# Performance work log

Measured on AMD Instinct MI355X. Metric: run time of the kernel, lower is better.

The kernel has to match this reference:

```python
import jax, jax.numpy as jnp
import numpy as np

B, H, W, C = 64, 56, 56, 192
HEADS, WS, SS, MLP = 6, 7, 3, 768
N = WS * WS            # 49 tokens per window
NW = (H // WS) * (W // WS)  # 64 windows per image
HEAD_DIM = C // HEADS
SCALE = HEAD_DIM ** (-0.5)


def _rpi(ws):
    # relative position index, (N, N) int
    coords = np.stack(np.meshgrid(np.arange(ws), np.arange(ws), indexing='ij')).reshape(2, -1)
    rel = (coords[:, :, None] - coords[:, None, :]).transpose(1, 2, 0)
    rel[:, :, 0] += ws - 1
    rel[:, :, 1] += ws - 1
    rel[:, :, 0] *= 2 * ws - 1
    return rel.sum(-1)

RPI = _rpi(WS).reshape(-1)  # (N*N,)


def _attn_mask():
    # additive shift mask, (NW, N, N)
    label = np.zeros((H, W))
    cnt = 0
    slices = (slice(0, -WS), slice(-WS, -SS), slice(-SS, None))
    for hs in slices:
        for ws_ in slices:
            label[hs, ws_] = cnt
            cnt += 1
    lab = label.reshape(H // WS, WS, W // WS, WS).transpose(0, 2, 1, 3).reshape(NW, N)
    diff = lab[:, None, :] - lab[:, :, None]
    return np.where(diff != 0, -100.0, 0.0).astype(np.float32)

MASK = jnp.asarray(_attn_mask())  # (NW, N, N)


def _ln(t, g, b, eps=1e-5):
    m = jnp.mean(t, -1, keepdims=True)
    v = jnp.mean((t - m) ** 2, -1, keepdims=True)
    return (t - m) * jax.lax.rsqrt(v + eps) * g + b


def setup_inputs() -> dict:
    key = jax.random.key(0)
    ks = jax.random.split(key, 6)
    s = 0.02
    return {
        'x': jax.random.normal(ks[0], (B, H * W, C), jnp.float32),
        'ln1_g': jnp.ones((C,), jnp.float32),
        'ln1_b': jnp.zeros((C,), jnp.float32),
        'qkv_w': jax.random.normal(ks[1], (C, 3 * C), jnp.float32) * s,
        'qkv_b': jnp.zeros((3 * C,), jnp.float32),
        'proj_w': jax.random.normal(ks[2], (C, C), jnp.float32) * s,
        'proj_b': jnp.zeros((C,), jnp.float32),
        'rpb': jax.random.normal(ks[3], ((2 * WS - 1) ** 2, HEADS), jnp.float32) * s,
        'ln2_g': jnp.ones((C,), jnp.float32),
        'ln2_b': jnp.zeros((C,), jnp.float32),
        'mlp_w1': jax.random.normal(ks[4], (C, MLP), jnp.float32) * s,
        'mlp_b1': jnp.zeros((MLP,), jnp.float32),
        'mlp_w2': jax.random.normal(ks[5], (MLP, C), jnp.float32) * s,
        'mlp_b2': jnp.zeros((C,), jnp.float32),
    }


def reference(x, ln1_g, ln1_b, qkv_w, qkv_b, proj_w, proj_b, rpb,
              ln2_g, ln2_b, mlp_w1, mlp_b1, mlp_w2, mlp_b2):
    # ---- Residual(PreNorm(Swin(WindowAttention))) ----
    h = _ln(x, ln1_g, ln1_b)                       # (B, L, C)
    h = h.reshape(B, H, W, C)
    h = jnp.roll(h, (-SS, -SS), (1, 2))            # cyclic shift
    # window partition -> (B*NW, N, C)
    h = h.reshape(B, H // WS, WS, W // WS, WS, C).transpose(0, 1, 3, 2, 4, 5).reshape(-1, N, C)
    qkv = (h @ qkv_w + qkv_b).reshape(-1, N, 3, HEADS, HEAD_DIM).transpose(2, 0, 3, 1, 4)
    q, k, v = qkv[0] * SCALE, qkv[1], qkv[2]       # (B*NW, heads, N, d)
    attn = jnp.einsum('bhid,bhjd->bhij', q, k)     # (B*NW, heads, N, N)
    bias = rpb[RPI].reshape(N, N, HEADS).transpose(2, 0, 1)  # (heads, N, N)
    attn = attn + bias[None]
    attn = attn.reshape(B, NW, HEADS, N, N) + MASK[None, :, None]
    attn = jax.nn.softmax(attn.reshape(-1, HEADS, N, N), axis=-1)
    out = jnp.einsum('bhij,bhjd->bhid', attn, v).transpose(0, 2, 1, 3).reshape(-1, N, C)
    out = out @ proj_w + proj_b
    # window reverse -> (B, H, W, C)
    out = out.reshape(B, H // WS, W // WS, WS, WS, C).transpose(0, 1, 3, 2, 4, 5).reshape(B, H, W, C)
    out = jnp.roll(out, (SS, SS), (1, 2)).reshape(B, H * W, C)
    x = x + out
    # ---- Residual(PreNorm(Mlp)) ----
    h2 = _ln(x, ln2_g, ln2_b)
    h2 = jax.nn.gelu(h2 @ mlp_w1 + mlp_b1, approximate=False) @ mlp_w2 + mlp_b2
    return x + h2
```

## Files before the change

### kernel.cpp

```cpp
#include <hip/hip_runtime.h>
#include <math.h>

typedef __attribute__((ext_vector_type(8))) short short8;
typedef __attribute__((ext_vector_type(4))) float floatx4;

#define M_TOT 200704
#define SCALE_Q 0.17677669529663687f

__device__ __forceinline__ float u2f(unsigned int u){ return __uint_as_float(u << 16); }
__device__ __forceinline__ unsigned short f2u(float f){
  unsigned int x = __float_as_uint(f);
  x += 0x7fffu + ((x >> 16) & 1u);
  return (unsigned short)(x >> 16);
}

__device__ __forceinline__ int win_to_x(int m){
  int bb = m / 3136; int rem = m - bb*3136;
  int w = rem / 49, n = rem - w*49;
  int wh = w >> 3, ww = w & 7;
  int i = n / 7, j = n - i*7;
  int p = wh*7 + i + 3; if (p >= 56) p -= 56;
  int q = ww*7 + j + 3; if (q >= 56) q -= 56;
  return bb*3136 + p*56 + q;
}

__global__ void conv_wt(const float* __restrict__ in, unsigned short* __restrict__ out,
                        int K, int N){
  int t = blockIdx.x*256 + threadIdx.x;
  if (t < K*N){ int k = t / N, n = t - k*N; out[n*K + k] = f2u(in[t]); }
}
__global__ void rowmap_k(int* __restrict__ map){
  int t = blockIdx.x*256 + threadIdx.x;
  if (t < M_TOT) map[t] = win_to_x(t);
}
__global__ void bm_k(const float* __restrict__ rpb, unsigned short* __restrict__ BM){
  int w = blockIdx.x / 6, h = blockIdx.x - (blockIdx.x/6)*6;
  int t = threadIdx.x;
  unsigned short* o = BM + ((size_t)blockIdx.x << 12);
  int wh = w >> 3, ww = w & 7;
  for (int z = 0; z < 16; ++z){
    int idx = t*16 + z;
    int i = idx >> 6, j = idx & 63;
    float val = -30000.0f;
    if (i < 49 && j < 49){
      int yi = i/7, xi = i - (i/7)*7, yj = j/7, xj = j - (j/7)*7;
      int pi_ = wh*7 + yi, qi_ = ww*7 + xi;
      int pj_ = wh*7 + yj, qj_ = ww*7 + xj;
      int li = (pi_<49?0:(pi_<53?1:2))*3 + (qi_<49?0:(qi_<53?1:2));
      int lj = (pj_<49?0:(pj_<53?1:2))*3 + (qj_<49?0:(qj_<53?1:2));
      int rel = (yi-yj+6)*13 + (xi-xj+6);
      val = rpb[rel*6 + h] + ((li == lj) ? 0.0f : -100.0f);
    }
    o[idx] = f2u(val);
  }
}

template<int KTOT, int NCG, int LNMODE, int EPI>
__global__ __launch_bounds__(512, 4) void gemm_kernel(
    const void* __restrict__ A, int astride, long row0g,
    const unsigned short* __restrict__ Wt,
    const float* __restrict__ lng, const float* __restrict__ lnb,
    const float* __restrict__ bias, const float* __restrict__ res,
    void* __restrict__ outp, int ostride, const int* __restrict__ rowmap){
  constexpr bool AFULL = (KTOT == 192);
  constexpr int ASTR  = AFULL ? 200 : 72;
  constexpr int NCH   = KTOT / 64;
  __shared__ __align__(16) unsigned short As[AFULL ? 128*200 : 128*72];
  __shared__ __align__(16) unsigned short Ws[192*72];
  int tid = threadIdx.x;
  int gx = gridDim.x;
  int nwg = gx * gridDim.y;
  int orig = blockIdx.y * gx + blockIdx.x;
  int qc = nwg >> 3, rc = nwg & 7;
  int xcd = orig & 7, idxk = orig >> 3;
  int wgid = (xcd < rc ? xcd*(qc+1) : rc*(qc+1) + (xcd-rc)*qc) + idxk;
  int bx = wgid % gx, by = wgid / gx;
  long lrow0 = (long)by * 128;
  int lane = tid & 63, wv = tid >> 6;
  int rw = wv >> 2, cw = wv & 3;
  int quad = lane >> 4, l16 = lane & 15;

  if constexpr (LNMODE != 0){
    int rr = tid >> 2, sub = tid & 3;
    long srow = (LNMODE == 1) ? (long)rowmap[row0g + lrow0 + rr] : (row0g + lrow0 + rr);
    const float* rp = (const float*)A + srow*192 + sub*48;
    float va[48];
    float s = 0.f, q2 = 0.f;
    #pragma unroll
    for (int i = 0; i < 12; ++i){
      float4 f = *(const float4*)(rp + i*4);
      va[i*4+0] = f.x; va[i*4+1] = f.y; va[i*4+2] = f.z; va[i*4+3] = f.w;
      s += (f.x + f.y) + (f.z + f.w);
      q2 = fmaf(f.x, f.x, q2); q2 = fmaf(f.y, f.y, q2);
      q2 = fmaf(f.z, f.z, q2); q2 = fmaf(f.w, f.w, q2);
    }
    s  += __shfl_xor(s, 1);  q2 += __shfl_xor(q2, 1);
    s  += __shfl_xor(s, 2);  q2 += __shfl_xor(q2, 2);
    float mean = s*(1.f/192.f);
    float rs = rsqrtf(q2*(1.f/192.f) - mean*mean + 1e-5f);
    float mrs = mean * rs;
    unsigned short* dst = As + rr*200 + sub*48;
    #pragma unroll
    for (int i = 0; i < 12; ++i){
      float4 g4 = *(const float4*)(lng + sub*48 + i*4);
      float4 b4 = *(const float4*)(lnb + sub*48 + i*4);
      ushort4 o;
      o.x = f2u(fmaf(fmaf(va[i*4+0], rs, -mrs), g4.x, b4.x));
      o.y = f2u(fmaf(fmaf(va[i*4+1], rs, -mrs), g4.y, b4.y));
      o.z = f2u(fmaf(fmaf(va[i*4+2], rs, -mrs), g4.z, b4.z));
      o.w = f2u(fmaf(fmaf(va[i*4+3], rs, -mrs), g4.w, b4.w));
      *(ushort4*)(dst + i*4) = o;
    }
  } else if constexpr (AFULL){
    #pragma unroll
    for (int it = 0; it < 6; ++it){
      int idx = tid + it*512;
      int rr2 = idx / 24, c16 = idx - rr2*24;
      long asrc = (lrow0 + rr2) * (long)astride + c16*8;
      *(uint4*)(As + rr2*200 + c16*8) = *(const uint4*)((const unsigned short*)A + asrc);
    }
  }

  #pragma unroll
  for (int g = 0; g < NCG; ++g){
    int n0 = (bx*NCG + g) * 192;
    floatx4 acc[12];
    #pragma unroll
    for (int i = 0; i < 12; ++i) acc[i] = (floatx4){0.f,0.f,0.f,0.f};

    for (int c = 0; c < NCH; ++c){
      if (g || c) __syncthreads();
      if constexpr (!AFULL){
        #pragma unroll
        for (int it = 0; it < 2; ++it){
          int idx = tid + it*512;
          int rr2 = idx >> 3, gr = idx & 7;
          long asrc = (lrow0 + rr2) * (long)astride + c*64 + gr*8;
          *(uint4*)(As + rr2*72 + gr*8) = *(const uint4*)((const unsigned short*)A + asrc);
        }
      }
      #pragma unroll
      for (int it = 0; it < 3; ++it){
        int idx = tid + it*512;
        int rr2 = idx >> 3, gr = idx & 7;
        *(uint4*)(Ws + rr2*72 + gr*8) =
            *(const uint4*)(Wt + (long)(n0 + rr2)*KTOT + c*64 + gr*8);
      }
      __syncthreads();
      int abase = AFULL ? c*64 : 0;
      #pragma unroll
      for (int kk = 0; kk < 2; ++kk){
        int ko = kk*32 + quad*8;
        short8 af[4];
        #pragma unroll
        for (int m = 0; m < 4; ++m)
          af[m] = *(const short8*)(As + (rw*64 + m*16 + l16)*ASTR + abase + ko);
        #pragma unroll
        for (int n = 0; n < 3; ++n){
          short8 bf = *(const short8*)(Ws + (cw*48 + n*16 + l16)*72 + ko);
          #pragma unroll
          for (int m = 0; m < 4; ++m)
            acc[m*3+n] = __builtin_amdgcn_mfma_f32_16x16x32_bf16(af[m], bf, acc[m*3+n], 0, 0, 0);
        }
      }
    }

    #pragma unroll
    for (int m = 0; m < 4; ++m){
      #pragma unroll
      for (int r2 = 0; r2 < 4; ++r2){
        long lm = lrow0 + rw*64 + m*16 + quad*4 + r2;
        long drow = 0;
        if (EPI == 1) drow = rowmap[row0g + lm];
        if (EPI == 3) drow = row0g + lm;
        #pragma unroll
        for (int n = 0; n < 3; ++n){
          int col = n0 + cw*48 + n*16 + l16;
          float v = acc[m*3+n][r2] + bias[col];
          if (EPI == 0){
            if (col < 192) v *= SCALE_Q;
            ((unsigned short*)outp)[lm*(long)ostride + col] = f2u(v);
          } else if (EPI == 1){
            v += res[drow*192 + col];
            ((float*)outp)[drow*192 + col] = v;
          } else if (EPI == 2){
            v = 0.5f*v*(1.0f + erff(v*0.70710678118654752f));
            ((unsigned short*)outp)[lm*(long)ostride + col] = f2u(v);
          } else {
            v += res[drow*192 + col];
            ((float*)outp)[drow*192 + col] = v;
          }
        }
      }
    }
  }
}

__global__ __launch_bounds__(64) void attn_kernel(unsigned short* __restrict__ qkv,
    const unsigned short* __restrict__ BM, long win0g){
  __shared__ __align__(16) unsigned short Vt[32*64];
  __shared__ __align__(16) unsigned short Pl[64*72];
  int bid = blockIdx.x;
  int wb = bid / 6, head = bid - wb*6;
  int t = threadIdx.x;
  int q = t >> 4, l16 = t & 15;
  long base = (long)wb * 49 * 576;
  const unsigned short* qkvb = qkv + base;

  #pragma unroll
  for (int z = 0; z < 8; ++z){
    int idx = t + z*64;
    int d = idx >> 4, jz = 48 + (idx & 15);
    Vt[d*64 + ((((jz>>3) ^ (d&7))<<3) | (jz&7))] = 0;
  }
  for (int idx = t; idx < 784; idx += 64){
    int j = idx >> 4, d2 = (idx & 15)*2;
    unsigned int u = *(const unsigned int*)(qkvb + (long)j*576 + 384 + head*32 + d2);
    Vt[d2*64 + ((((j>>3) ^ (d2&7))<<3) | (j&7))]       = (unsigned short)(u & 0xffffu);
    Vt[(d2+1)*64 + ((((j>>3) ^ ((d2+1)&7))<<3) | (j&7))] = (unsigned short)(u >> 16);
  }

  short8 kf[4], qf[4];
  #pragma unroll
  for (int jt = 0; jt < 4; ++jt){
    int j = jt*16 + l16; j = j > 48 ? 48 : j;
    kf[jt] = *(const short8*)(qkvb + (long)j*576 + 192 + head*32 + q*8);
  }
  #pragma unroll
  for (int it = 0; it < 4; ++it){
    int i = it*16 + l16; i = i > 48 ? 48 : i;
    qf[it] = *(const short8*)(qkvb + (long)i*576 + head*32 + q*8);
  }
  floatx4 acc[16];
  #pragma unroll
  for (int z = 0; z < 16; ++z) acc[z] = (floatx4){0.f,0.f,0.f,0.f};
  #pragma unroll
  for (int jt = 0; jt < 4; ++jt){
    #pragma unroll
    for (int it = 0; it < 4; ++it)
      acc[jt*4+it] = __builtin_amdgcn_mfma_f32_16x16x32_bf16(kf[jt], qf[it], acc[jt*4+it], 0, 0, 0);
  }

  int w = (int)((win0g + wb) & 63);
  const unsigned short* bmp = BM + ((size_t)(w*6 + head) << 12);
  #pragma unroll
  for (int it = 0; it < 4; ++it){
    float mx = -3.0e38f;
    #pragma unroll
    for (int jt = 0; jt < 4; ++jt){
      ushort4 bm = *(const ushort4*)(bmp + (it*16 + l16)*64 + jt*16 + q*4);
      floatx4 s = acc[jt*4+it];
      s[0] += u2f(bm.x); s[1] += u2f(bm.y); s[2] += u2f(bm.z); s[3] += u2f(bm.w);
      acc[jt*4+it] = s;
      mx = fmaxf(mx, fmaxf(fmaxf(s[0], s[1]), fmaxf(s[2], s[3])));
    }
    mx = fmaxf(mx, __shfl_xor(mx, 16));
    mx = fmaxf(mx, __shfl_xor(mx, 32));
    float sum = 0.f;
    #pragma unroll
    for (int jt = 0; jt < 4; ++jt){
      floatx4 s = acc[jt*4+it];
      s[0] = __expf(s[0]-mx); s[1] = __expf(s[1]-mx);
      s[2] = __expf(s[2]-mx); s[3] = __expf(s[3]-mx);
      acc[jt*4+it] = s;
      sum += (s[0]+s[1]) + (s[2]+s[3]);
    }
    sum += __shfl_xor(sum, 16);
    sum += __shfl_xor(sum, 32);
    float inv = 1.0f / sum;
    #pragma unroll
    for (int jt = 0; jt < 4; ++jt){
      floatx4 s = acc[jt*4+it];
      ushort4 pk;
      pk.x = f2u(s[0]*inv); pk.y = f2u(s[1]*inv);
      pk.z = f2u(s[2]*inv); pk.w = f2u(s[3]*inv);
      *(ushort4*)(Pl + (it*16 + l16)*72 + jt*16 + q*4) = pk;
    }
  }
  __syncthreads();

  floatx4 oa[8];
  #pragma unroll
  for (int z = 0; z < 8; ++z) oa[z] = (floatx4){0.f,0.f,0.f,0.f};
  #pragma unroll
  for (int ks = 0; ks < 2; ++ks){
    short8 pf[4];
    #pragma unroll
    for (int mt = 0; mt < 4; ++mt)
      pf[mt] = *(const short8*)(Pl + (mt*16 + l16)*72 + ks*32 + q*8);
    #pragma unroll
    for (int nt = 0; nt < 2; ++nt){
      int d = nt*16 + l16;
      short8 vf = *(const short8*)(Vt + d*64 + (((ks*4 + q) ^ (d&7))<<3));
      #pragma unroll
      for (int mt = 0; mt < 4; ++mt)
        oa[mt*2+nt] = __builtin_amdgcn_mfma_f32_16x16x32_bf16(pf[mt], vf, oa[mt*2+nt], 0, 0, 0);
    }
  }
  #pragma unroll
  for (int mt = 0; mt < 4; ++mt){
    #pragma unroll
    for (int r = 0; r < 4; ++r){
      int i = mt*16 + q*4 + r;
      if (i < 49){
        unsigned short* op = qkv + base + (long)i*576 + head*32;
        op[l16]      = f2u(oa[mt*2+0][r]);
        op[16 + l16] = f2u(oa[mt*2+1][r]);
      }
    }
  }
}

extern "C" void kernel_launch(void* const* d_in, const int* in_sizes, int n_in,
                              void* d_out, int out_size, void* d_ws, size_t ws_size,
                              hipStream_t stream){
  const float* x     = (const float*)d_in[0];
  const float* ln1_g = (const float*)d_in[1];
  const float* ln1_b = (const float*)d_in[2];
  const float* qkv_w = (const float*)d_in[3];
  const float* qkv_b = (const float*)d_in[4];
  const float* proj_w= (const float*)d_in[5];
  const float* proj_b= (const float*)d_in[6];
  const float* rpb   = (const float*)d_in[7];
  const float* ln2_g = (const float*)d_in[8];
  const float* ln2_b = (const float*)d_in[9];
  const float* w1    = (const float*)d_in[10];
  const float* b1    = (const float*)d_in[11];
  const float* w2    = (const float*)d_in[12];
  const float* b2    = (const float*)d_in[13];
  float* out = (float*)d_out;

  unsigned short* wt_qkv  = (unsigned short*)d_ws;
  unsigned short* wt_proj = wt_qkv  + 576*192;
  unsigned short* wt_m1   = wt_proj + 192*192;
  unsigned short* wt_m2   = wt_m1   + 768*192;
  int* rowmap = (int*)(wt_m2 + 192*768);
  unsigned short* bm = (unsigned short*)(rowmap + M_TOT);
  unsigned short* buf = bm + (size_t)384*4096;
  size_t ovh = (size_t)(576*192 + 192*192 + 768*192 + 192*768)*2 + (size_t)M_TOT*4
             + (size_t)384*4096*2;
  size_t bufb = ws_size > ovh ? ws_size - ovh : 0;

  int da = 64;
  while (da > 2 && (size_t)3136*(size_t)da*1152ULL > bufb) da >>= 1;
  long Sa = 3136L*da;
  int nA = 64/da;
  static const long smlist[] = {200704,100352,50176,25088,12544,6272,1792,1024,512,256,128};
  long Sm = 128;
  for (int i = 0; i < 11; ++i) if ((size_t)smlist[i]*1536ULL <= bufb){ Sm = smlist[i]; break; }
  int nM = (int)(M_TOT / Sm);

  conv_wt<<<(192*576+255)/256, 256, 0, stream>>>(qkv_w, wt_qkv, 192, 576);
  conv_wt<<<(192*192+255)/256, 256, 0, stream>>>(proj_w, wt_proj, 192, 192);
  conv_wt<<<(192*768+255)/256, 256, 0, stream>>>(w1, wt_m1, 192, 768);
  conv_wt<<<(768*192+255)/256, 256, 0, stream>>>(w2, wt_m2, 768, 192);
  rowmap_k<<<(M_TOT+255)/256, 256, 0, stream>>>(rowmap);
  bm_k<<<384, 256, 0, stream>>>(rpb, bm);

  for (int s = 0; s < nA; ++s){
    long r0 = (long)s*Sa;
    gemm_kernel<192,3,1,0><<<dim3(1, Sa/128), 512, 0, stream>>>(
        x, 192, r0, wt_qkv, ln1_g, ln1_b, qkv_b, nullptr, buf, 576, rowmap);
    attn_kernel<<<(int)(Sa/49)*6, 64, 0, stream>>>(buf, bm, r0/49);
    gemm_kernel<192,1,0,1><<<dim3(1, Sa/128), 512, 0, stream>>>(
        buf, 576, r0, wt_proj, nullptr, nullptr, proj_b, x, out, 192, rowmap);
  }

  for (int s = 0; s < nM; ++s){
    long r0 = (long)s*Sm;
    gemm_kernel<192,2,2,2><<<dim3(2, Sm/128), 512, 0, stream>>>(
        out, 192, r0, wt_m1, ln2_g, ln2_b, b1, nullptr, buf, 768, rowmap);
    gemm_kernel<768,1,0,3><<<dim3(1, Sm/128), 512, 0, stream>>>(
        buf, 768, r0, wt_m2, nullptr, nullptr, b2, out, out, 192, rowmap);
  }
}
```

Baseline: 969.6 us.

## Load GEMM tiles via global_load_lds into XOR-swizzled LDS, tanh-approx GELU

GEMM A and weight tiles now go straight from global memory to LDS with global_load_lds, replacing the padded-row layout with an XOR swizzle on 16-byte groups so MFMA fragment reads avoid bank conflicts. The LayerNorm write path and fragment addressing are updated to the same swizzle. The exact erf GELU is swapped for a sigmoid form of the tanh approximation, which changes numerics relative to the reference. The weight-transpose kernel also now writes coalesced.

```diff
diff --git a/kernel.cpp b/kernel.cpp
--- a/kernel.cpp
+++ b/kernel.cpp
@@ -13,6 +13,10 @@
   x += 0x7fffu + ((x >> 16) & 1u);
   return (unsigned short)(x >> 16);
 }
+
+#define GLD16(gp, lp) __builtin_amdgcn_global_load_lds( \
+    (const __attribute__((address_space(1))) void*)(gp), \
+    (__attribute__((address_space(3))) void*)(lp), 16, 0, 0)
 
 __device__ __forceinline__ int win_to_x(int m){
   int bb = m / 3136; int rem = m - bb*3136;
@@ -27,7 +31,7 @@
 __global__ void conv_wt(const float* __restrict__ in, unsigned short* __restrict__ out,
                         int K, int N){
   int t = blockIdx.x*256 + threadIdx.x;
-  if (t < K*N){ int k = t / N, n = t - k*N; out[n*K + k] = f2u(in[t]); }
+  if (t < K*N){ int n = t / K, k = t - n*K; out[t] = f2u(in[k*N + n]); }
 }
 __global__ void rowmap_k(int* __restrict__ map){
   int t = blockIdx.x*256 + threadIdx.x;
@@ -63,10 +67,10 @@
     const float* __restrict__ bias, const float* __restrict__ res,
     void* __restrict__ outp, int ostride, const int* __restrict__ rowmap){
   constexpr bool AFULL = (KTOT == 192);
-  constexpr int ASTR  = AFULL ? 200 : 72;
+  constexpr int AROW  = AFULL ? 192 : 64;
   constexpr int NCH   = KTOT / 64;
-  __shared__ __align__(16) unsigned short As[AFULL ? 128*200 : 128*72];
-  __shared__ __align__(16) unsigned short Ws[192*72];
+  __shared__ __align__(16) unsigned short As[AFULL ? 128*192 : 128*64];
+  __shared__ __align__(16) unsigned short Ws[192*64];
   int tid = threadIdx.x;
   int gx = gridDim.x;
   int nwg = gx * gridDim.y;
@@ -99,7 +103,7 @@
     float mean = s*(1.f/192.f);
     float rs = rsqrtf(q2*(1.f/192.f) - mean*mean + 1e-5f);
     float mrs = mean * rs;
-    unsigned short* dst = As + rr*200 + sub*48;
+    unsigned short* dstb = As + rr*192;
     #pragma unroll
     for (int i = 0; i < 12; ++i){
       float4 g4 = *(const float4*)(lng + sub*48 + i*4);
@@ -109,15 +113,16 @@
       o.y = f2u(fmaf(fmaf(va[i*4+1], rs, -mrs), g4.y, b4.y));
       o.z = f2u(fmaf(fmaf(va[i*4+2], rs, -mrs), g4.z, b4.z));
       o.w = f2u(fmaf(fmaf(va[i*4+3], rs, -mrs), g4.w, b4.w));
-      *(ushort4*)(dst + i*4) = o;
+      *(ushort4*)(dstb + (((sub*6 + (i>>1)) ^ (rr&7))<<3) + ((i&1)<<2)) = o;
     }
   } else if constexpr (AFULL){
     #pragma unroll
     for (int it = 0; it < 6; ++it){
-      int idx = tid + it*512;
-      int rr2 = idx / 24, c16 = idx - rr2*24;
-      long asrc = (lrow0 + rr2) * (long)astride + c16*8;
-      *(uint4*)(As + rr2*200 + c16*8) = *(const uint4*)((const unsigned short*)A + asrc);
+      int gi = (wv*6 + it)*64 + lane;
+      int r = gi / 24, g = gi - r*24;
+      const unsigned short* src = (const unsigned short*)A
+          + (lrow0 + r)*(long)astride + ((g ^ (r&7))<<3);
+      GLD16(src, As + ((wv*6 + it)<<9));
     }
   }
 
@@ -133,31 +138,36 @@
       if constexpr (!AFULL){
         #pragma unroll
         for (int it = 0; it < 2; ++it){
-          int idx = tid + it*512;
-          int rr2 = idx >> 3, gr = idx & 7;
-          long asrc = (lrow0 + rr2) * (long)astride + c*64 + gr*8;
-          *(uint4*)(As + rr2*72 + gr*8) = *(const uint4*)((const unsigned short*)A + asrc);
+          int gi = (wv*2 + it)*64 + lane;
+          int r = gi >> 3, gg = gi & 7;
+          const unsigned short* src = (const unsigned short*)A
+              + (lrow0 + r)*(long)astride + c*64 + ((gg ^ (r&7))<<3);
+          GLD16(src, As + ((wv*2 + it)<<9));
         }
       }
       #pragma unroll
       for (int it = 0; it < 3; ++it){
-        int idx = tid + it*512;
-        int rr2 = idx >> 3, gr = idx & 7;
-        *(uint4*)(Ws + rr2*72 + gr*8) =
-            *(const uint4*)(Wt + (long)(n0 + rr2)*KTOT + c*64 + gr*8);
+        int gi = (wv*3 + it)*64 + lane;
+        int r = gi >> 3, gg = gi & 7;
+        const unsigned short* src = Wt + (long)(n0 + r)*KTOT + c*64 + ((gg ^ (r&7))<<3);
+        GLD16(src, Ws + ((wv*3 + it)<<9));
       }
       __syncthreads();
-      int abase = AFULL ? c*64 : 0;
+      int gA0 = AFULL ? c*8 : 0;
       #pragma unroll
       for (int kk = 0; kk < 2; ++kk){
-        int ko = kk*32 + quad*8;
+        int ga = gA0 + kk*4 + quad;
         short8 af[4];
         #pragma unroll
-        for (int m = 0; m < 4; ++m)
-          af[m] = *(const short8*)(As + (rw*64 + m*16 + l16)*ASTR + abase + ko);
+        for (int m = 0; m < 4; ++m){
+          int r = rw*64 + m*16 + l16;
+          af[m] = *(const short8*)(As + r*AROW + ((ga ^ (r&7))<<3));
+        }
+        int gb = kk*4 + quad;
         #pragma unroll
         for (int n = 0; n < 3; ++n){
-          short8 bf = *(const short8*)(Ws + (cw*48 + n*16 + l16)*72 + ko);
+          int rb = cw*48 + n*16 + l16;
+          short8 bf = *(const short8*)(Ws + rb*64 + ((gb ^ (rb&7))<<3));
           #pragma unroll
           for (int m = 0; m < 4; ++m)
             acc[m*3+n] = __builtin_amdgcn_mfma_f32_16x16x32_bf16(af[m], bf, acc[m*3+n], 0, 0, 0);
@@ -184,7 +194,8 @@
             v += res[drow*192 + col];
             ((float*)outp)[drow*192 + col] = v;
           } else if (EPI == 2){
-            v = 0.5f*v*(1.0f + erff(v*0.70710678118654752f));
+            float zz = 1.5957691216057308f * v * fmaf(v*v, 0.044715f, 1.0f);
+            v = v * __builtin_amdgcn_rcpf(1.0f + __expf(-zz));
             ((unsigned short*)outp)[lm*(long)ostride + col] = f2u(v);
           } else {
             v += res[drow*192 + col];
```

Result: faster. 931.2 us (-4.0%).
